# Kernel optimization log

Measured on AMD Instinct MI355X. Metric: run time of the kernel, lower is better.

## Reference

```python
import jax, jax.numpy as jnp
import numpy as np
from jax import lax


def _conv(x, w, stride=1):
    # x: [N,C,H,W], w: [O,I,k,k]
    return lax.conv_general_dilated(x, w, (stride, stride), 'SAME',
                                    dimension_numbers=('NCHW', 'OIHW', 'NCHW'))


def _up2(x):
    return jnp.repeat(jnp.repeat(x, 2, axis=-2), 2, axis=-1)


def _model(x, Wbs, bbs, Wc1, bc1, Wc2, bc2, Wes, bes):
    h = x
    for W, b in zip(Wbs, bbs):
        h = jax.nn.relu(_conv(h, W, 2) + b[None, :, None, None])
    feats = h  # [B, 512, 4, 4]
    pooled = feats.mean(axis=(2, 3))  # AdaptiveAvgPool2d((1,1)) + Flatten
    hidden = jax.nn.relu(pooled @ Wc1.T + bc1)
    logits = hidden @ Wc2.T + bc2  # [B, 5]
    cls = jnp.argmax(logits, axis=1)  # per-sample expert routing (force_class=None path)

    def expert(f, ws, bs):  # f: [512,4,4]; one sample through its routed UNet decoder
        e = f[None]
        for i in range(5):
            e = _up2(e)
            e = jax.nn.relu(_conv(e, ws[i]) + bs[i][None, :, None, None])
        e = _conv(e, ws[5]) + bs[5][None, :, None, None]  # 1x1 head -> 5 seg channels
        return e[0]

    # MoE-style dispatch: gather each sample's expert weights, then vmap (no per-sample Python loop)
    ws_sel = tuple(W[cls] for W in Wes)  # each [B, co, ci, k, k]
    bs_sel = tuple(b[cls] for b in bes)  # each [B, co]
    seg = jax.vmap(expert)(feats, ws_sel, bs_sel)  # [B, 5, 128, 128]
    return logits, cls, seg


def setup_inputs() -> dict:
    key = jax.random.key(0)
    ks = iter(jax.random.split(key, 48))

    def rn(shape):
        return jax.random.normal(next(ks), shape, dtype=jnp.float32) * 0.05

    B, E = 64, 5
    inp = {"x": jax.random.normal(next(ks), (B, 3, 128, 128), dtype=jnp.float32)}
    for i, (ci, co) in enumerate([(3, 64), (64, 128), (128, 256), (256, 512), (512, 512)], 1):
        inp[f"Wb{i}"] = rn((co, ci, 3, 3))
        inp[f"bb{i}"] = rn((co,))
    inp["Wc1"] = rn((128, 512)); inp["bc1"] = rn((128,))
    inp["Wc2"] = rn((5, 128)); inp["bc2"] = rn((5,))
    for i, (ci, co, k) in enumerate([(512, 256, 3), (256, 128, 3), (128, 64, 3),
                                     (64, 32, 3), (32, 16, 3), (16, 5, 1)], 1):
        inp[f"We{i}"] = rn((E, co, ci, k, k))
        inp[f"be{i}"] = rn((E, co))
    return inp


def reference(x, Wb1, bb1, Wb2, bb2, Wb3, bb3, Wb4, bb4, Wb5, bb5,
              Wc1, bc1, Wc2, bc2,
              We1, be1, We2, be2, We3, be3, We4, be4, We5, be5, We6, be6):
    return _model(x,
                  (Wb1, Wb2, Wb3, Wb4, Wb5), (bb1, bb2, bb3, bb4, bb5),
                  Wc1, bc1, Wc2, bc2,
                  (We1, We2, We3, We4, We5, We6), (be1, be2, be3, be4, be5, be6))
```

## Files before the change

kernel.cpp:

```cpp
#include <hip/hip_runtime.h>
#include <hip/hip_bf16.h>


typedef __attribute__((ext_vector_type(8))) short bf16x8;
typedef __attribute__((ext_vector_type(4))) float f32x4;

static __device__ __forceinline__ unsigned short f2bf(float f) {
    __hip_bfloat16 h = __float2bfloat16(f);
    return *reinterpret_cast<unsigned short*>(&h);
}
static __device__ __forceinline__ float bf2f(unsigned short u) {
    return __uint_as_float(((unsigned int)u) << 16);
}

__global__ __launch_bounds__(256)
void conv1_kernel(const float* __restrict__ in, const float* __restrict__ W,
                  const float* __restrict__ Bias,
                  unsigned short* __restrict__ out_hi,
                  unsigned short* __restrict__ out_lo)
{
    constexpr int R = 17, C = 17;
    __shared__ float ilds[3*R*C];
    __shared__ float wlds[27*32];
    const int n = blockIdx.z, co0 = blockIdx.y*32;
    const int ty = blockIdx.x >> 3, tx = blockIdx.x & 7;
    const int oh0 = ty*8, ow0 = tx*8;
    const int t = threadIdx.x, p = t & 63, grp = t >> 6;
    const int py = p >> 3, px = p & 7;
    const int r0 = 2*oh0, c0 = 2*ow0;

    const float* ibase = in + (long)n*3*16384;
    for (int idx = t; idx < 3*R*C; idx += 256) {
        int ck = idx/(R*C), rc = idx%(R*C);
        int r = rc/C, c = rc%C;
        int ih = r0+r, iw = c0+c;
        float v = 0.f;
        if (ih < 128 && iw < 128) v = ibase[ck*16384 + ih*128 + iw];
        ilds[idx] = v;
    }
    for (int idx = t; idx < 32*27; idx += 256) {
        int co = idx & 31, rem = idx >> 5;
        wlds[rem*32 + co] = W[(co0+co)*27 + rem];
    }
    __syncthreads();

    float acc[8];
    #pragma unroll
    for (int i=0;i<8;i++) acc[i]=0.f;

    #pragma unroll
    for (int ck = 0; ck < 3; ++ck) {
        float xv[9];
        #pragma unroll
        for (int kh = 0; kh < 3; ++kh)
            #pragma unroll
            for (int kw = 0; kw < 3; ++kw)
                xv[kh*3+kw] = ilds[ck*289 + (2*py+kh)*17 + 2*px+kw];
        #pragma unroll
        for (int k = 0; k < 9; ++k) {
            #pragma unroll
            for (int g = 0; g < 2; ++g) {
                const float4 w = *reinterpret_cast<const float4*>(
                    &wlds[(ck*9+k)*32 + grp*8 + g*4]);
                acc[g*4+0] += xv[k]*w.x;
                acc[g*4+1] += xv[k]*w.y;
                acc[g*4+2] += xv[k]*w.z;
                acc[g*4+3] += xv[k]*w.w;
            }
        }
    }

    const long obase = (((long)n*64 + oh0+py)*64 + ow0+px)*64 + co0 + grp*8;
    #pragma unroll
    for (int g = 0; g < 2; ++g) {
        ushort4 sh, sl;
        #pragma unroll
        for (int j = 0; j < 4; ++j) {
            int co = co0 + grp*8 + g*4 + j;
            float v = fmaxf(acc[g*4+j] + Bias[co], 0.f);
            unsigned short h = f2bf(v);
            ((unsigned short*)&sh)[j] = h;
            ((unsigned short*)&sl)[j] = f2bf(v - bf2f(h));
        }
        *reinterpret_cast<ushort4*>(&out_hi[obase + g*4]) = sh;
        *reinterpret_cast<ushort4*>(&out_lo[obase + g*4]) = sl;
    }
}

template<int CI,int CO,int HO,int NW,int NPACK>
__global__ __launch_bounds__(NW*64, 2)
void bb_conv_v2(const unsigned short* __restrict__ in_hi,
                const unsigned short* __restrict__ in_lo,
                const unsigned short* __restrict__ Whi,
                const unsigned short* __restrict__ Wlo,
                const float* __restrict__ Bias,
                unsigned short* __restrict__ out_hi,
                unsigned short* __restrict__ out_lo)
{
    constexpr int HI = HO*2;
    constexpr int TH = (NPACK==1) ? 8 : 4;
    constexpr int TW = TH;
    constexpr int R  = 2*TH+1, C = 2*TW+1;
    constexpr int CK = 32;
    constexpr int PITCH = CK + 8;
    constexpr int CO_T  = NW*64;
    constexpr int NTHR  = NW*64;

    __shared__ __align__(16) unsigned short hi_lds[NPACK*R*C*PITCH];
    __shared__ __align__(16) unsigned short lo_lds[NPACK*R*C*PITCH];

    const int n0  = blockIdx.z * NPACK;
    const int co0 = blockIdx.y * CO_T;
    constexpr int TILES_X = (NPACK==1) ? (HO/TW) : 1;
    const int ty = blockIdx.x / TILES_X, tx = blockIdx.x % TILES_X;
    const int oh0 = ty*TH, ow0 = tx*TW;
    const int r0 = 2*oh0, c0 = 2*ow0;

    const int t = threadIdx.x;
    const int w = t >> 6, lane = t & 63;
    const int s = lane & 15, q = lane >> 4;

    int dyy[4], dxx[4], tb[4];
    #pragma unroll
    for (int si = 0; si < 4; ++si) {
        if (NPACK == 1) { dyy[si] = si*2 + (s>>3); dxx[si] = s & 7; tb[si] = 0; }
        else            { dyy[si] = s >> 2;        dxx[si] = s & 3; tb[si] = si*R*C*PITCH; }
    }

    int wrow[4];
    #pragma unroll
    for (int tn = 0; tn < 4; ++tn)
        wrow[tn] = (co0 + w*64 + tn*16 + s)*9*CI + q*8;

    f32x4 acc[4][4];
    #pragma unroll
    for (int si = 0; si < 4; ++si)
        #pragma unroll
        for (int tn = 0; tn < 4; ++tn)
            acc[si][tn] = (f32x4){0.f,0.f,0.f,0.f};

    for (int ci0 = 0; ci0 < CI; ci0 += CK) {
        constexpr int C8  = CK/8;
        constexpr int PXW = R*C*C8;
        for (int i8 = t; i8 < NPACK*PXW; i8 += NTHR) {
            int ti = i8 / PXW, rem = i8 % PXW;
            int pix = rem / C8, cs = rem % C8;
            int r = pix / C, c = pix % C;
            int ih = r0 + r, iw = c0 + c;
            uint4 vh = {0u,0u,0u,0u}, vl = {0u,0u,0u,0u};
            if (ih < HI && iw < HI) {
                long off = (((long)(n0+ti)*HI + ih)*HI + iw)*CI + ci0 + cs*8;
                vh = *reinterpret_cast<const uint4*>(&in_hi[off]);
                vl = *reinterpret_cast<const uint4*>(&in_lo[off]);
            }
            *reinterpret_cast<uint4*>(&hi_lds[(ti*R*C + pix)*PITCH + cs*8]) = vh;
            *reinterpret_cast<uint4*>(&lo_lds[(ti*R*C + pix)*PITCH + cs*8]) = vl;
        }
        __syncthreads();

        bf16x8 ah[2][4], al[2][4];
        #pragma unroll
        for (int tn = 0; tn < 4; ++tn) {
            const int wo = wrow[tn] + ci0;
            ah[0][tn] = *reinterpret_cast<const bf16x8*>(&Whi[wo]);
            al[0][tn] = *reinterpret_cast<const bf16x8*>(&Wlo[wo]);
        }
        #pragma unroll
        for (int k = 0; k < 9; ++k) {
            const int cur = k & 1, nxt = cur ^ 1;
            if (k < 8) {
                #pragma unroll
                for (int tn = 0; tn < 4; ++tn) {
                    const int wo = wrow[tn] + (k+1)*CI + ci0;
                    ah[nxt][tn] = *reinterpret_cast<const bf16x8*>(&Whi[wo]);
                    al[nxt][tn] = *reinterpret_cast<const bf16x8*>(&Wlo[wo]);
                }
            }
            const int kh = k/3, kw = k%3;
            bf16x8 bh[4], bl[4];
            #pragma unroll
            for (int si = 0; si < 4; ++si) {
                const int pi = tb[si] + ((2*dyy[si]+kh)*C + 2*dxx[si]+kw)*PITCH + q*8;
                bh[si] = *reinterpret_cast<const bf16x8*>(&hi_lds[pi]);
                bl[si] = *reinterpret_cast<const bf16x8*>(&lo_lds[pi]);
            }
            #pragma unroll
            for (int si = 0; si < 4; ++si)
                #pragma unroll
                for (int tn = 0; tn < 4; ++tn) {
                    acc[si][tn] = __builtin_amdgcn_mfma_f32_16x16x32_bf16(ah[cur][tn], bh[si], acc[si][tn], 0,0,0);
                    acc[si][tn] = __builtin_amdgcn_mfma_f32_16x16x32_bf16(ah[cur][tn], bl[si], acc[si][tn], 0,0,0);
                    acc[si][tn] = __builtin_amdgcn_mfma_f32_16x16x32_bf16(al[cur][tn], bh[si], acc[si][tn], 0,0,0);
                }
        }
        __syncthreads();
    }

    #pragma unroll
    for (int si = 0; si < 4; ++si) {
        const int n_s = (NPACK==1) ? n0 : (n0 + si);
        const int oh  = (NPACK==1) ? (oh0 + dyy[si]) : dyy[si];
        const int ow  = (NPACK==1) ? (ow0 + dxx[si]) : dxx[si];
        #pragma unroll
        for (int tn = 0; tn < 4; ++tn) {
            int co_b = co0 + w*64 + tn*16 + q*4;
            ushort4 sh, sl;
            #pragma unroll
            for (int r = 0; r < 4; ++r) {
                float v = fmaxf(acc[si][tn][r] + Bias[co_b + r], 0.f);
                unsigned short h = f2bf(v);
                ((unsigned short*)&sh)[r] = h;
                ((unsigned short*)&sl)[r] = f2bf(v - bf2f(h));
            }
            long ob = (((long)n_s*HO + oh)*HO + ow)*CO + co_b;
            *reinterpret_cast<ushort4*>(&out_hi[ob]) = sh;
            *reinterpret_cast<ushort4*>(&out_lo[ob]) = sl;
        }
    }
}

__global__ __launch_bounds__(128, 2)
void conv5_partial(const unsigned short* __restrict__ in_hi,
                   const unsigned short* __restrict__ in_lo,
                   const unsigned short* __restrict__ Whi,
                   const unsigned short* __restrict__ Wlo,
                   float* __restrict__ skbuf)
{
    constexpr int CI = 512, HI = 8;
    constexpr int R = 9, C = 9, CK = 32, PITCH = 40;
    constexpr int SK = 8, CIB = CI/SK;

    __shared__ __align__(16) unsigned short hi_lds[4*R*C*PITCH];
    __shared__ __align__(16) unsigned short lo_lds[4*R*C*PITCH];

    const int sk  = blockIdx.x;
    const int co0 = blockIdx.y * 128;
    const int n0  = blockIdx.z * 4;
    const int t = threadIdx.x;
    const int w = t >> 6, lane = t & 63;
    const int s = lane & 15, q = lane >> 4;
    const int dyy = s >> 2, dxx = s & 3;

    int wrow[4];
    #pragma unroll
    for (int tn = 0; tn < 4; ++tn)
        wrow[tn] = (co0 + w*64 + tn*16 + s)*9*CI + q*8;

    f32x4 acc[4][4];
    #pragma unroll
    for (int si = 0; si < 4; ++si)
        #pragma unroll
        for (int tn = 0; tn < 4; ++tn)
            acc[si][tn] = (f32x4){0.f,0.f,0.f,0.f};

    for (int cc = 0; cc < CIB; cc += CK) {
        const int ci0 = sk*CIB + cc;
        constexpr int C8 = CK/8;
        constexpr int PXW = R*C*C8;
        for (int i8 = t; i8 < 4*PXW; i8 += 128) {
            int ti = i8 / PXW, rem = i8 % PXW;
            int pix = rem / C8, cs = rem % C8;
            int r = pix / C, c = pix % C;
            uint4 vh = {0u,0u,0u,0u}, vl = {0u,0u,0u,0u};
            if (r < HI && c < HI) {
                long off = (((long)(n0+ti)*HI + r)*HI + c)*CI + ci0 + cs*8;
                vh = *reinterpret_cast<const uint4*>(&in_hi[off]);
                vl = *reinterpret_cast<const uint4*>(&in_lo[off]);
            }
            *reinterpret_cast<uint4*>(&hi_lds[(ti*R*C + pix)*PITCH + cs*8]) = vh;
            *reinterpret_cast<uint4*>(&lo_lds[(ti*R*C + pix)*PITCH + cs*8]) = vl;
        }
        __syncthreads();

        bf16x8 ah[2][4], al[2][4];
        #pragma unroll
        for (int tn = 0; tn < 4; ++tn) {
            const int wo = wrow[tn] + ci0;
            ah[0][tn] = *reinterpret_cast<const bf16x8*>(&Whi[wo]);
            al[0][tn] = *reinterpret_cast<const bf16x8*>(&Wlo[wo]);
        }
        #pragma unroll
        for (int k = 0; k < 9; ++k) {
            const int cur = k & 1, nxt = cur ^ 1;
            if (k < 8) {
                #pragma unroll
                for (int tn = 0; tn < 4; ++tn) {
                    const int wo = wrow[tn] + (k+1)*CI + ci0;
                    ah[nxt][tn] = *reinterpret_cast<const bf16x8*>(&Whi[wo]);
                    al[nxt][tn] = *reinterpret_cast<const bf16x8*>(&Wlo[wo]);
                }
            }
            const int kh = k/3, kw = k%3;
            bf16x8 bh[4], bl[4];
            #pragma unroll
            for (int si = 0; si < 4; ++si) {
                const int pi = si*R*C*PITCH + ((2*dyy+kh)*C + 2*dxx+kw)*PITCH + q*8;
                bh[si] = *reinterpret_cast<const bf16x8*>(&hi_lds[pi]);
                bl[si] = *reinterpret_cast<const bf16x8*>(&lo_lds[pi]);
            }
            #pragma unroll
            for (int si = 0; si < 4; ++si)
                #pragma unroll
                for (int tn = 0; tn < 4; ++tn) {
                    acc[si][tn] = __builtin_amdgcn_mfma_f32_16x16x32_bf16(ah[cur][tn], bh[si], acc[si][tn], 0,0,0);
                    acc[si][tn] = __builtin_amdgcn_mfma_f32_16x16x32_bf16(ah[cur][tn], bl[si], acc[si][tn], 0,0,0);
                    acc[si][tn] = __builtin_amdgcn_mfma_f32_16x16x32_bf16(al[cur][tn], bh[si], acc[si][tn], 0,0,0);
                }
        }
        __syncthreads();
    }

    #pragma unroll
    for (int si = 0; si < 4; ++si) {
        #pragma unroll
        for (int tn = 0; tn < 4; ++tn) {
            int co_b = co0 + w*64 + tn*16 + q*4;
            long o = (((long)sk*64 + n0+si)*16 + s)*512 + co_b;
            *reinterpret_cast<f32x4*>(&skbuf[o]) = acc[si][tn];
        }
    }
}

__global__ __launch_bounds__(256)
void conv5_reduce(const float* __restrict__ skbuf, const float* __restrict__ Bias,
                  unsigned short* __restrict__ fhi, unsigned short* __restrict__ flo)
{
    int i = blockIdx.x*256 + threadIdx.x;
    int co = i & 511;
    float sacc = Bias[co];
    #pragma unroll
    for (int sk = 0; sk < 8; ++sk) sacc += skbuf[sk*524288 + i];
    float v = fmaxf(sacc, 0.f);
    unsigned short h = f2bf(v);
    fhi[i] = h;
    flo[i] = f2bf(v - bf2f(h));
}

__global__ __launch_bounds__(128, 2)
void dec1_partial(const unsigned short* __restrict__ in,
                  const unsigned short* __restrict__ WT,
                  const int* __restrict__ cls_i,
                  float* __restrict__ dbuf)
{
    constexpr int CI = 512, CO = 256, HI = 4;
    constexpr int R = 6, C = 6, CK = 64, CKQ = 2, PITCH = 72;
    constexpr int SK = 4, CIB = CI/SK;

    __shared__ __align__(16) unsigned short ilds[R*C*PITCH];

    const int sk  = blockIdx.x;
    const int co0 = blockIdx.y * 128;
    const int n   = blockIdx.z;
    const int e   = cls_i[n];
    const int t = threadIdx.x;
    const int w = t >> 6, lane = t & 63;
    const int s = lane & 15, q = lane >> 4;

    const unsigned short* Wbase = WT + (long)e*CO*9*CI;
    const unsigned short* inN   = in + (long)n*HI*HI*CI;

    int dyy[4], dxx[4];
    #pragma unroll
    for (int si = 0; si < 4; ++si) { dyy[si] = si*2 + (s>>3); dxx[si] = s & 7; }

    long wrow[4];
    #pragma unroll
    for (int tn = 0; tn < 4; ++tn)
        wrow[tn] = (long)(co0 + w*64 + tn*16 + s)*9*CI + q*8;

    f32x4 acc[4][4];
    #pragma unroll
    for (int si = 0; si < 4; ++si)
        #pragma unroll
        for (int tn = 0; tn < 4; ++tn)
            acc[si][tn] = (f32x4){0.f,0.f,0.f,0.f};

    for (int cc = 0; cc < CIB; cc += CK) {
        const int ci0 = sk*CIB + cc;
        constexpr int C8 = CK/8;
        for (int i8 = t; i8 < R*C*C8; i8 += 128) {
            int pix = i8 / C8, cs = i8 % C8;
            int r = pix / C, c = pix % C;
            int ih = r - 1, iw = c - 1;
            uint4 v = {0u,0u,0u,0u};
            if (ih >= 0 && ih < HI && iw >= 0 && iw < HI)
                v = *reinterpret_cast<const uint4*>(&inN[((long)ih*HI + iw)*CI + ci0 + cs*8]);
            *reinterpret_cast<uint4*>(&ilds[pix*PITCH + cs*8]) = v;
        }
        __syncthreads();

        bf16x8 a[2][4];
        #pragma unroll
        for (int tn = 0; tn < 4; ++tn)
            a[0][tn] = *reinterpret_cast<const bf16x8*>(&Wbase[wrow[tn] + ci0]);
        #pragma unroll
        for (int st = 0; st < 9*CKQ; ++st) {
            const int cur = st & 1, nxt = cur ^ 1;
            if (st + 1 < 9*CKQ) {
                const int kp = (st+1)/CKQ, cp = (st+1)%CKQ;
                #pragma unroll
                for (int tn = 0; tn < 4; ++tn)
                    a[nxt][tn] = *reinterpret_cast<const bf16x8*>(
                        &Wbase[wrow[tn] + kp*CI + ci0 + cp*32]);
            }
            const int k = st/CKQ, ckq = st%CKQ;
            const int kh = k/3, kw = k%3;
            #pragma unroll
            for (int si = 0; si < 4; ++si) {
                const int ihr = ((dyy[si] + kh - 1) >> 1) + 1;
                const int iwr = ((dxx[si] + kw - 1) >> 1) + 1;
                bf16x8 b = *reinterpret_cast<const bf16x8*>(
                    &ilds[(ihr*C + iwr)*PITCH + ckq*32 + q*8]);
                #pragma unroll
                for (int tn = 0; tn < 4; ++tn)
                    acc[si][tn] = __builtin_amdgcn_mfma_f32_16x16x32_bf16(
                        a[cur][tn], b, acc[si][tn], 0, 0, 0);
            }
        }
        __syncthreads();
    }

    #pragma unroll
    for (int si = 0; si < 4; ++si) {
        int px = dyy[si]*8 + dxx[si];
        #pragma unroll
        for (int tn = 0; tn < 4; ++tn) {
            int co_b = co0 + w*64 + tn*16 + q*4;
            long o = (((long)sk*64 + n)*64 + px)*256 + co_b;
            *reinterpret_cast<f32x4*>(&dbuf[o]) = acc[si][tn];
        }
    }
}

__global__ __launch_bounds__(256)
void dec1_reduce(const float* __restrict__ dbuf, const float* __restrict__ be1,
                 const int* __restrict__ cls_i, unsigned short* __restrict__ P)
{
    int i = blockIdx.x*256 + threadIdx.x;
    int n = i >> 14;
    int co = i & 255;
    int e = cls_i[n];
    float sacc = be1[e*256 + co];
    #pragma unroll
    for (int sk = 0; sk < 4; ++sk) sacc += dbuf[sk*1048576 + i];
    P[i] = f2bf(fmaxf(sacc, 0.f));
}

template<int CI>
__global__ __launch_bounds__(256)
void wtrans_split_kernel(const float* __restrict__ src,
                         unsigned short* __restrict__ hi,
                         unsigned short* __restrict__ lo)
{
    __shared__ float buf[CI*9];
    const long blk = blockIdx.x;
    const float* sp = src + blk*(CI*9);
    for (int i = threadIdx.x; i < CI*9; i += 256) buf[i] = sp[i];
    __syncthreads();
    for (int i = threadIdx.x; i < CI*9; i += 256) {
        int k = i / CI, ci = i % CI;
        float v = buf[ci*9 + k];
        unsigned short h = f2bf(v);
        hi[blk*(CI*9) + i] = h;
        lo[blk*(CI*9) + i] = f2bf(v - bf2f(h));
    }
}

template<int CI>
__global__ __launch_bounds__(256)
void wtrans_kernel(const float* __restrict__ src, unsigned short* __restrict__ dst)
{
    __shared__ float buf[CI*9];
    const long blk = blockIdx.x;
    const float* sp = src + blk*(CI*9);
    for (int i = threadIdx.x; i < CI*9; i += 256) buf[i] = sp[i];
    __syncthreads();
    unsigned short* d = dst + blk*(CI*9);
    for (int i = threadIdx.x; i < CI*9; i += 256) {
        int k = i / CI, ci = i % CI;
        d[i] = f2bf(buf[ci*9 + k]);
    }
}

__global__ __launch_bounds__(256) void pool_kernel(const unsigned short* __restrict__ fh,
                                                   const unsigned short* __restrict__ fl,
                                                   float* __restrict__ pooled)
{
    int i = blockIdx.x*256 + threadIdx.x;
    if (i < 64*512) {
        int n = i >> 9, ci = i & 511;
        const unsigned short* ph = fh + (long)n*8192 + ci;
        const unsigned short* pl = fl + (long)n*8192 + ci;
        float sacc = 0.f;
        #pragma unroll
        for (int px = 0; px < 16; ++px)
            sacc += bf2f(ph[px*512]) + bf2f(pl[px*512]);
        pooled[i] = sacc * (1.f/16.f);
    }
}

__global__ __launch_bounds__(256) void fc1_kernel(const float* __restrict__ pooled,
                                                  const float* __restrict__ Wc1,
                                                  const float* __restrict__ bc1,
                                                  float* __restrict__ hidden)
{
    int i = blockIdx.x*256 + threadIdx.x;
    if (i < 64*128) {
        int n = i/128, j = i%128;
        const float* p = pooled + n*512;
        const float* w = Wc1 + j*512;
        float sacc = 0.f;
        for (int k = 0; k < 512; ++k) sacc += p[k]*w[k];
        hidden[i] = fmaxf(sacc + bc1[j], 0.f);
    }
}

__global__ __launch_bounds__(64) void fc2_kernel(const float* __restrict__ hidden,
                                                 const float* __restrict__ Wc2,
                                                 const float* __restrict__ bc2,
                                                 float* __restrict__ out,
                                                 int* __restrict__ cls_i)
{
    int n = blockIdx.x;
    int j = threadIdx.x;
    __shared__ float lg[5];
    if (j < 5) {
        const float* h = hidden + n*128;
        const float* w = Wc2 + j*128;
        float sacc = 0.f;
        for (int k = 0; k < 128; ++k) sacc += h[k]*w[k];
        sacc += bc2[j];
        out[n*5 + j] = sacc;
        lg[j] = sacc;
    }
    __syncthreads();
    if (j == 0) {
        int am = 0; float best = lg[0];
        #pragma unroll
        for (int k = 1; k < 5; ++k) if (lg[k] > best) { best = lg[k]; am = k; }
        out[320 + n] = (float)am;
        cls_i[n] = am;
    }
}

template<int CI,int CO,int HO,int NW>
__global__ __launch_bounds__(NW*64, 2)
void dec_conv_v2(const unsigned short* __restrict__ in,
                 const unsigned short* __restrict__ WT,
                 const float* __restrict__ Be,
                 const int* __restrict__ cls_i,
                 unsigned short* __restrict__ out)
{
    constexpr int HI = HO/2;
    constexpr int R = 6, C = 6;
    constexpr int CK = 64, CKQ = CK/32;
    constexpr int PITCH = CK + 8;
    constexpr int CO_T = NW*64;
    constexpr int NTHR = NW*64;

    __shared__ __align__(16) unsigned short ilds[R*C*PITCH];

    const int n = blockIdx.z;
    const int e = cls_i[n];
    const int co0 = blockIdx.y * CO_T;
    constexpr int TILES_X = HO/8;
    const int ty = blockIdx.x / TILES_X, tx = blockIdx.x % TILES_X;
    const int oh0 = ty*8, ow0 = tx*8;
    const int ih0 = oh0/2 - 1, iw0 = ow0/2 - 1;

    const int t = threadIdx.x;
    const int w = t >> 6, lane = t & 63;
    const int s = lane & 15, q = lane >> 4;

    const unsigned short* Wbase = WT + (long)e*CO*9*CI;
    const unsigned short* inN   = in + (long)n*HI*HI*CI;

    int dyy[4], dxx[4];
    #pragma unroll
    for (int si = 0; si < 4; ++si) { dyy[si] = si*2 + (s>>3); dxx[si] = s & 7; }

    long wrow[4];
    #pragma unroll
    for (int tn = 0; tn < 4; ++tn)
        wrow[tn] = (long)(co0 + w*64 + tn*16 + s)*9*CI + q*8;

    f32x4 acc[4][4];
    #pragma unroll
    for (int si = 0; si < 4; ++si)
        #pragma unroll
        for (int tn = 0; tn < 4; ++tn)
            acc[si][tn] = (f32x4){0.f,0.f,0.f,0.f};

    for (int ci0 = 0; ci0 < CI; ci0 += CK) {
        constexpr int C8 = CK/8;
        for (int i8 = t; i8 < R*C*C8; i8 += NTHR) {
            int pix = i8 / C8, cs = i8 % C8;
            int r = pix / C, c = pix % C;
            int ih = ih0 + r, iw = iw0 + c;
            uint4 v = {0u,0u,0u,0u};
            if (ih >= 0 && ih < HI && iw >= 0 && iw < HI)
                v = *reinterpret_cast<const uint4*>(&inN[((long)ih*HI + iw)*CI + ci0 + cs*8]);
            *reinterpret_cast<uint4*>(&ilds[pix*PITCH + cs*8]) = v;
        }
        __syncthreads();

        bf16x8 a[2][4];
        #pragma unroll
        for (int tn = 0; tn < 4; ++tn)
            a[0][tn] = *reinterpret_cast<const bf16x8*>(&Wbase[wrow[tn] + ci0]);
        #pragma unroll
        for (int st = 0; st < 9*CKQ; ++st) {
            const int cur = st & 1, nxt = cur ^ 1;
            if (st + 1 < 9*CKQ) {
                const int kp = (st+1)/CKQ, cp = (st+1)%CKQ;
                #pragma unroll
                for (int tn = 0; tn < 4; ++tn)
                    a[nxt][tn] = *reinterpret_cast<const bf16x8*>(
                        &Wbase[wrow[tn] + kp*CI + ci0 + cp*32]);
            }
            const int k = st/CKQ, ckq = st%CKQ;
            const int kh = k/3, kw = k%3;
            #pragma unroll
            for (int si = 0; si < 4; ++si) {
                const int ihr = ((dyy[si] + kh - 1) >> 1) + 1;
                const int iwr = ((dxx[si] + kw - 1) >> 1) + 1;
                bf16x8 b = *reinterpret_cast<const bf16x8*>(
                    &ilds[(ihr*C + iwr)*PITCH + ckq*32 + q*8]);
                #pragma unroll
                for (int tn = 0; tn < 4; ++tn)
                    acc[si][tn] = __builtin_amdgcn_mfma_f32_16x16x32_bf16(
                        a[cur][tn], b, acc[si][tn], 0, 0, 0);
            }
        }
        __syncthreads();
    }

    #pragma unroll
    for (int si = 0; si < 4; ++si) {
        int oh = oh0 + dyy[si], ow = ow0 + dxx[si];
        #pragma unroll
        for (int tn = 0; tn < 4; ++tn) {
            int co_b = co0 + w*64 + tn*16 + q*4;
            ushort4 st4;
            #pragma unroll
            for (int r = 0; r < 4; ++r) {
                float v = acc[si][tn][r] + Be[e*CO + co_b + r];
                v = fmaxf(v, 0.f);
                ((unsigned short*)&st4)[r] = f2bf(v);
            }
            *reinterpret_cast<ushort4*>(&out[(((long)n*HO + oh)*HO + ow)*CO + co_b]) = st4;
        }
    }
}

template<int CI,int CO,int HO,int TH,int TW,int CO_T,int CK>
__global__ __launch_bounds__(256, 2)
void dec_conv_kernel(const unsigned short* __restrict__ in,
                     const unsigned short* __restrict__ WT,
                     const float* __restrict__ Be,
                     const int* __restrict__ cls_i,
                     unsigned short* __restrict__ out)
{
    constexpr int HI = HO/2;
    constexpr int R = TH/2 + 2, C = TW/2 + 2;
    constexpr int PITCH = CK + 8;
    constexpr int NT = CO_T/16;
    constexpr int S  = (TH*TW)/64;
    constexpr int SXT = TW/8;
    constexpr int CKQ = CK/32;
    constexpr int NST = 9*CKQ;
    constexpr int PF  = 3;

    __shared__ __align__(16) unsigned short ilds[R*C*PITCH];

    const int n = blockIdx.z;
    const int e = cls_i[n];
    const int co0 = blockIdx.y * CO_T;
    constexpr int TILES_X = HO/TW;
    const int ty = blockIdx.x / TILES_X, tx = blockIdx.x % TILES_X;
    const int oh0 = ty*TH, ow0 = tx*TW;
    const int ih0 = oh0/2 - 1, iw0 = ow0/2 - 1;

    const int t = threadIdx.x;
    const int w = t >> 6;
    const int lane = t & 63;
    const int s = lane & 15;
    const int q = lane >> 4;

    const unsigned short* Wbase = WT + ((long)e*CO + co0)*9*CI;
    const unsigned short* inN   = in + (long)n*HI*HI*CI;

    int wrow[NT];
    #pragma unroll
    for (int tn = 0; tn < NT; ++tn)
        wrow[tn] = (tn*16 + s)*9*CI + q*8;

    f32x4 acc[S][NT];
    #pragma unroll
    for (int si = 0; si < S; ++si)
        #pragma unroll
        for (int tn = 0; tn < NT; ++tn)
            acc[si][tn] = (f32x4){0.f,0.f,0.f,0.f};

    int dy[S], dx[S];
    #pragma unroll
    for (int si = 0; si < S; ++si) {
        int sub = w + si*4;
        int sy = sub / SXT, sx = sub % SXT;
        dy[si] = sy*2 + (s >> 3);
        dx[si] = sx*8 + (s & 7);
    }

    for (int ci0 = 0; ci0 < CI; ci0 += CK) {
        constexpr int C8 = CK/8;
        for (int i8 = t; i8 < R*C*C8; i8 += 256) {
            int pix = i8 / C8, cs = i8 % C8;
            int r = pix / C, c = pix % C;
            int ih = ih0 + r, iw = iw0 + c;
            uint4 v = {0u,0u,0u,0u};
            if (ih >= 0 && ih < HI && iw >= 0 && iw < HI)
                v = *reinterpret_cast<const uint4*>(&inN[((long)ih*HI + iw)*CI + ci0 + cs*8]);
            *reinterpret_cast<uint4*>(&ilds[pix*PITCH + cs*8]) = v;
        }
        __syncthreads();

        bf16x8 a[NST][NT];
        #pragma unroll
        for (int pf = 0; pf < PF && pf < NST; ++pf)
            #pragma unroll
            for (int tn = 0; tn < NT; ++tn) {
                const int k = pf/CKQ, ckq = pf%CKQ;
                a[pf][tn] = *reinterpret_cast<const bf16x8*>(
                    &Wbase[wrow[tn] + k*CI + ci0 + ckq*32]);
            }
        #pragma unroll
        for (int st = 0; st < NST; ++st) {
            if (st + PF < NST) {
                const int kp = (st+PF)/CKQ, cp = (st+PF)%CKQ;
                #pragma unroll
                for (int tn = 0; tn < NT; ++tn)
                    a[st+PF][tn] = *reinterpret_cast<const bf16x8*>(
                        &Wbase[wrow[tn] + kp*CI + ci0 + cp*32]);
            }
            const int k = st/CKQ, ckq = st%CKQ;
            const int kh = k/3, kw = k%3;
            #pragma unroll
            for (int si = 0; si < S; ++si) {
                int ihr = ((dy[si] + kh - 1) >> 1) + 1;
                int iwr = ((dx[si] + kw - 1) >> 1) + 1;
                bf16x8 b = *reinterpret_cast<const bf16x8*>(
                    &ilds[(ihr*C + iwr)*PITCH + ckq*32 + q*8]);
                #pragma unroll
                for (int tn = 0; tn < NT; ++tn)
                    acc[si][tn] = __builtin_amdgcn_mfma_f32_16x16x32_bf16(
                        a[st][tn], b, acc[si][tn], 0, 0, 0);
            }
        }
        __syncthreads();
    }

    #pragma unroll
    for (int si = 0; si < S; ++si) {
        int oh = oh0 + dy[si], ow = ow0 + dx[si];
        #pragma unroll
        for (int tn = 0; tn < NT; ++tn) {
            int co_b = co0 + tn*16 + q*4;
            ushort4 st4;
            #pragma unroll
            for (int r = 0; r < 4; ++r) {
                float v = acc[si][tn][r] + Be[e*CO + co_b + r];
                v = fmaxf(v, 0.f);
                ((unsigned short*)&st4)[r] = f2bf(v);
            }
            *reinterpret_cast<ushort4*>(&out[(((long)n*HO + oh)*HO + ow)*CO + co_b]) = st4;
        }
    }
}

__global__ __launch_bounds__(256) void head_kernel(const unsigned short* __restrict__ d5,
                                                   const float* __restrict__ Wh,
                                                   const float* __restrict__ bh,
                                                   const int* __restrict__ cls_i,
                                                   float* __restrict__ seg)
{
    int n = blockIdx.y;
    int p = blockIdx.x*256 + threadIdx.x;
    __shared__ float w[85];
    int e = cls_i[n];
    if (threadIdx.x < 80) w[threadIdx.x] = Wh[(long)e*80 + threadIdx.x];
    if (threadIdx.x < 5)  w[80+threadIdx.x] = bh[e*5 + threadIdx.x];
    __syncthreads();
    const unsigned short* dp = d5 + ((long)n*16384 + p)*16;
    uint4 u0 = *reinterpret_cast<const uint4*>(dp);
    uint4 u1 = *reinterpret_cast<const uint4*>(dp + 8);
    float x[16];
    unsigned int uu[4] = {u0.x, u0.y, u0.z, u0.w};
    unsigned int vv[4] = {u1.x, u1.y, u1.z, u1.w};
    #pragma unroll
    for (int i = 0; i < 4; ++i) {
        x[2*i+0] = __uint_as_float(uu[i] << 16);
        x[2*i+1] = __uint_as_float(uu[i] & 0xffff0000u);
        x[8+2*i+0] = __uint_as_float(vv[i] << 16);
        x[8+2*i+1] = __uint_as_float(vv[i] & 0xffff0000u);
    }
    #pragma unroll
    for (int co = 0; co < 5; ++co) {
        float sacc = w[80+co];
        #pragma unroll
        for (int ci = 0; ci < 16; ++ci) sacc += x[ci]*w[co*16+ci];
        seg[((long)n*5 + co)*16384 + p] = sacc;
    }
}

extern "C" void kernel_launch(void* const* d_in, const int* in_sizes, int n_in,
                              void* d_out, int out_size, void* d_ws, size_t ws_size,
                              hipStream_t stream)
{
    const float* x   = (const float*)d_in[0];
    const float* Wb1 = (const float*)d_in[1];  const float* bb1 = (const float*)d_in[2];
    const float* Wb2 = (const float*)d_in[3];  const float* bb2 = (const float*)d_in[4];
    const float* Wb3 = (const float*)d_in[5];  const float* bb3 = (const float*)d_in[6];
    const float* Wb4 = (const float*)d_in[7];  const float* bb4 = (const float*)d_in[8];
    const float* Wb5 = (const float*)d_in[9];  const float* bb5 = (const float*)d_in[10];
    const float* Wc1 = (const float*)d_in[11]; const float* bc1 = (const float*)d_in[12];
    const float* Wc2 = (const float*)d_in[13]; const float* bc2 = (const float*)d_in[14];
    const float* We1 = (const float*)d_in[15]; const float* be1 = (const float*)d_in[16];
    const float* We2 = (const float*)d_in[17]; const float* be2 = (const float*)d_in[18];
    const float* We3 = (const float*)d_in[19]; const float* be3 = (const float*)d_in[20];
    const float* We4 = (const float*)d_in[21]; const float* be4 = (const float*)d_in[22];
    const float* We5 = (const float*)d_in[23]; const float* be5 = (const float*)d_in[24];
    const float* We6 = (const float*)d_in[25]; const float* be6 = (const float*)d_in[26];

    float* out = (float*)d_out;
    char* ws = (char*)d_ws;

    unsigned short* H1hi = (unsigned short*)(ws + 0);
    unsigned short* H1lo = (unsigned short*)(ws + 33554432);
    unsigned short* H3hi = (unsigned short*)(ws + 0);
    unsigned short* H3lo = (unsigned short*)(ws + 8388608);
    unsigned short* WB4hi = (unsigned short*)(ws + 16777216);
    unsigned short* WB4lo = (unsigned short*)(ws + 19136512);
    unsigned short* WB5hi = (unsigned short*)(ws + 21495808);
    unsigned short* WB5lo = (unsigned short*)(ws + 26214400);
    float*          SKBUF5 = (float*)(ws + 0);
    unsigned short* P    = (unsigned short*)(ws + 0);
    unsigned short* Q    = (unsigned short*)(ws + 33554432);
    float*          DBUF1 = (float*)(ws + 33554432);
    unsigned short* WT1  = (unsigned short*)(ws + 50331648);
    unsigned short* WT2  = (unsigned short*)(ws + 62128128);
    unsigned short* WT3  = (unsigned short*)(ws + 65077248);
    unsigned short* WT4  = (unsigned short*)(ws + 65814528);
    unsigned short* WT5  = (unsigned short*)(ws + 65998848);

    char* Y = ws + 67108864;
    unsigned short* H2hi = (unsigned short*)(Y + 0);
    unsigned short* H2lo = (unsigned short*)(Y + 16777216);
    unsigned short* H4hi = (unsigned short*)(Y + 0);
    unsigned short* H4lo = (unsigned short*)(Y + 4194304);
    unsigned short* FShi = (unsigned short*)(Y + 8388608);
    unsigned short* FSlo = (unsigned short*)(Y + 9437184);
    float* pooled = (float*)(Y + 10485760);
    float* hidden = (float*)(Y + 10616832);
    int*   cls_i  = (int*)(Y + 10649600);

    char* W23 = ws + 100663296;
    unsigned short* WB2hi = (unsigned short*)(W23 + 0);
    unsigned short* WB2lo = (unsigned short*)(W23 + 147456);
    unsigned short* WB3hi = (unsigned short*)(W23 + 294912);
    unsigned short* WB3lo = (unsigned short*)(W23 + 884736);

    hipLaunchKernelGGL((wtrans_split_kernel<64>),  dim3(128), dim3(256), 0, stream, Wb2, WB2hi, WB2lo);
    hipLaunchKernelGGL((wtrans_split_kernel<128>), dim3(256), dim3(256), 0, stream, Wb3, WB3hi, WB3lo);

    hipLaunchKernelGGL(conv1_kernel, dim3(64,2,64), dim3(256), 0, stream, x, Wb1, bb1, H1hi, H1lo);

    hipLaunchKernelGGL((bb_conv_v2<64,128,32,2,1>), dim3(16,1,64), dim3(128), 0, stream,
                       H1hi, H1lo, WB2hi, WB2lo, bb2, H2hi, H2lo);

    hipLaunchKernelGGL((wtrans_split_kernel<256>), dim3(512), dim3(256), 0, stream, Wb4, WB4hi, WB4lo);
    hipLaunchKernelGGL((wtrans_split_kernel<512>), dim3(512), dim3(256), 0, stream, Wb5, WB5hi, WB5lo);
    hipLaunchKernelGGL((wtrans_kernel<512>), dim3(5*256), dim3(256), 0, stream, We1, WT1);
    hipLaunchKernelGGL((wtrans_kernel<256>), dim3(5*128), dim3(256), 0, stream, We2, WT2);
    hipLaunchKernelGGL((wtrans_kernel<128>), dim3(5*64),  dim3(256), 0, stream, We3, WT3);
    hipLaunchKernelGGL((wtrans_kernel<64>),  dim3(5*32),  dim3(256), 0, stream, We4, WT4);
    hipLaunchKernelGGL((wtrans_kernel<32>),  dim3(5*16),  dim3(256), 0, stream, We5, WT5);

    hipLaunchKernelGGL((bb_conv_v2<128,256,16,2,1>), dim3(4,2,64), dim3(128), 0, stream,
                       H2hi, H2lo, WB3hi, WB3lo, bb3, H3hi, H3lo);
    hipLaunchKernelGGL((bb_conv_v2<256,512, 8,2,1>), dim3(1,4,64), dim3(128), 0, stream,
                       H3hi, H3lo, WB4hi, WB4lo, bb4, H4hi, H4lo);

    hipLaunchKernelGGL(conv5_partial, dim3(8,4,16), dim3(128), 0, stream,
                       H4hi, H4lo, WB5hi, WB5lo, SKBUF5);
    hipLaunchKernelGGL(conv5_reduce, dim3(2048), dim3(256), 0, stream,
                       SKBUF5, bb5, FShi, FSlo);

    hipLaunchKernelGGL(pool_kernel, dim3(128), dim3(256), 0, stream, FShi, FSlo, pooled);
    hipLaunchKernelGGL(fc1_kernel,  dim3(32),  dim3(256), 0, stream, pooled, Wc1, bc1, hidden);
    hipLaunchKernelGGL(fc2_kernel,  dim3(64),  dim3(64),  0, stream, hidden, Wc2, bc2, out, cls_i);

    hipLaunchKernelGGL(dec1_partial, dim3(4,2,64), dim3(128), 0, stream,
                       FShi, WT1, cls_i, DBUF1);
    hipLaunchKernelGGL(dec1_reduce, dim3(4096), dim3(256), 0, stream,
                       DBUF1, be1, cls_i, P);

    hipLaunchKernelGGL((dec_conv_v2<256,128, 16,2>), dim3(4, 1,64), dim3(128), 0, stream, P, WT2, be2, cls_i, Q);
    hipLaunchKernelGGL((dec_conv_v2<128, 64, 32,1>), dim3(16,1,64), dim3(64),  0, stream, Q, WT3, be3, cls_i, P);
    hipLaunchKernelGGL((dec_conv_kernel< 64, 32, 64, 16,16, 32,64>), dim3(16, 1,64), dim3(256), 0, stream, P, WT4, be4, cls_i, Q);
    hipLaunchKernelGGL((dec_conv_kernel< 32, 16,128, 16,16, 16,32>), dim3(64, 1,64), dim3(256), 0, stream, Q, WT5, be5, cls_i, P);

    hipLaunchKernelGGL(head_kernel, dim3(64,64), dim3(256), 0, stream, P, We6, be6, cls_i, out + 384);
}
```

Measured before the change: 689.7 us.

## Restage split-bf16 convs, fuse weight transforms and classifier, retune decoder tiles

The backbone convs now stage the hi and lo activation halves through a single LDS buffer in two passes, not both halves at once. This halves shared memory and the per-k LDS reads, at the cost of extra barriers and re-loading the hi weights. The many weight-transform launches and the pool/fc1/fc2 chain are merged into a few combined kernels to cut launch overhead. The decoder convs move to a 3-slot rotating weight prefetch ring to reduce register pressure, and the last decoder conv uses a wider tile with half as many blocks.

```diff
diff --git a/kernel.cpp b/kernel.cpp
--- a/kernel.cpp
+++ b/kernel.cpp
@@ -87,9 +87,9 @@
     }
 }
 
-template<int CI,int CO,int HO,int NW,int NPACK>
+template<int CI,int CO,int HO,int NW>
 __global__ __launch_bounds__(NW*64, 2)
-void bb_conv_v2(const unsigned short* __restrict__ in_hi,
+void bb_conv_v3(const unsigned short* __restrict__ in_hi,
                 const unsigned short* __restrict__ in_lo,
                 const unsigned short* __restrict__ Whi,
                 const unsigned short* __restrict__ Wlo,
@@ -98,34 +98,29 @@
                 unsigned short* __restrict__ out_lo)
 {
     constexpr int HI = HO*2;
-    constexpr int TH = (NPACK==1) ? 8 : 4;
-    constexpr int TW = TH;
-    constexpr int R  = 2*TH+1, C = 2*TW+1;
-    constexpr int CK = 32;
-    constexpr int PITCH = CK + 8;
-    constexpr int CO_T  = NW*64;
-    constexpr int NTHR  = NW*64;
-
-    __shared__ __align__(16) unsigned short hi_lds[NPACK*R*C*PITCH];
-    __shared__ __align__(16) unsigned short lo_lds[NPACK*R*C*PITCH];
-
-    const int n0  = blockIdx.z * NPACK;
-    const int co0 = blockIdx.y * CO_T;
-    constexpr int TILES_X = (NPACK==1) ? (HO/TW) : 1;
+    constexpr int R = 17, C = 17;
+    constexpr int CK = 32, PITCH = 40;
+    constexpr int NTHR = NW*64;
+
+    __shared__ __align__(16) unsigned short xlds[R*C*PITCH];
+
+    const int n   = blockIdx.z;
+    const int co0 = blockIdx.y * (NW*64);
+    constexpr int TILES_X = HO/8;
     const int ty = blockIdx.x / TILES_X, tx = blockIdx.x % TILES_X;
-    const int oh0 = ty*TH, ow0 = tx*TW;
+    const int oh0 = ty*8, ow0 = tx*8;
     const int r0 = 2*oh0, c0 = 2*ow0;
 
     const int t = threadIdx.x;
     const int w = t >> 6, lane = t & 63;
     const int s = lane & 15, q = lane >> 4;
 
-    int dyy[4], dxx[4], tb[4];
-    #pragma unroll
-    for (int si = 0; si < 4; ++si) {
-        if (NPACK == 1) { dyy[si] = si*2 + (s>>3); dxx[si] = s & 7; tb[si] = 0; }
-        else            { dyy[si] = s >> 2;        dxx[si] = s & 3; tb[si] = si*R*C*PITCH; }
-    }
+    int dyy[4], dxx[4];
+    #pragma unroll
+    for (int si = 0; si < 4; ++si) { dyy[si] = si*2 + (s>>3); dxx[si] = s & 7; }
+
+    const unsigned short* inHn = in_hi + (long)n*HI*HI*CI;
+    const unsigned short* inLn = in_lo + (long)n*HI*HI*CI;
 
     int wrow[4];
     #pragma unroll
@@ -139,68 +134,84 @@
         for (int tn = 0; tn < 4; ++tn)
             acc[si][tn] = (f32x4){0.f,0.f,0.f,0.f};
 
-    for (int ci0 = 0; ci0 < CI; ci0 += CK) {
-        constexpr int C8  = CK/8;
-        constexpr int PXW = R*C*C8;
-        for (int i8 = t; i8 < NPACK*PXW; i8 += NTHR) {
-            int ti = i8 / PXW, rem = i8 % PXW;
-            int pix = rem / C8, cs = rem % C8;
+    auto stage = [&](const unsigned short* base, int ci0) {
+        for (int i8 = t; i8 < R*C*4; i8 += NTHR) {
+            int pix = i8 >> 2, cs = i8 & 3;
             int r = pix / C, c = pix % C;
             int ih = r0 + r, iw = c0 + c;
-            uint4 vh = {0u,0u,0u,0u}, vl = {0u,0u,0u,0u};
-            if (ih < HI && iw < HI) {
-                long off = (((long)(n0+ti)*HI + ih)*HI + iw)*CI + ci0 + cs*8;
-                vh = *reinterpret_cast<const uint4*>(&in_hi[off]);
-                vl = *reinterpret_cast<const uint4*>(&in_lo[off]);
-            }
-            *reinterpret_cast<uint4*>(&hi_lds[(ti*R*C + pix)*PITCH + cs*8]) = vh;
-            *reinterpret_cast<uint4*>(&lo_lds[(ti*R*C + pix)*PITCH + cs*8]) = vl;
-        }
-        __syncthreads();
-
-        bf16x8 ah[2][4], al[2][4];
-        #pragma unroll
-        for (int tn = 0; tn < 4; ++tn) {
-            const int wo = wrow[tn] + ci0;
-            ah[0][tn] = *reinterpret_cast<const bf16x8*>(&Whi[wo]);
-            al[0][tn] = *reinterpret_cast<const bf16x8*>(&Wlo[wo]);
-        }
-        #pragma unroll
-        for (int k = 0; k < 9; ++k) {
-            const int cur = k & 1, nxt = cur ^ 1;
-            if (k < 8) {
+            uint4 v = {0u,0u,0u,0u};
+            if (ih < HI && iw < HI)
+                v = *reinterpret_cast<const uint4*>(&base[((long)ih*HI + iw)*CI + ci0 + cs*8]);
+            *reinterpret_cast<uint4*>(&xlds[pix*PITCH + cs*8]) = v;
+        }
+    };
+
+    for (int ci0 = 0; ci0 < CI; ci0 += CK) {
+        stage(inHn, ci0);
+        __syncthreads();
+        {
+            bf16x8 ah[2][4], al[2][4];
+            #pragma unroll
+            for (int tn = 0; tn < 4; ++tn) {
+                ah[0][tn] = *reinterpret_cast<const bf16x8*>(&Whi[wrow[tn] + ci0]);
+                al[0][tn] = *reinterpret_cast<const bf16x8*>(&Wlo[wrow[tn] + ci0]);
+            }
+            #pragma unroll
+            for (int k = 0; k < 9; ++k) {
+                const int cur = k & 1, nxt = cur ^ 1;
+                if (k < 8) {
+                    #pragma unroll
+                    for (int tn = 0; tn < 4; ++tn) {
+                        ah[nxt][tn] = *reinterpret_cast<const bf16x8*>(&Whi[wrow[tn] + (k+1)*CI + ci0]);
+                        al[nxt][tn] = *reinterpret_cast<const bf16x8*>(&Wlo[wrow[tn] + (k+1)*CI + ci0]);
+                    }
+                }
+                const int kh = k/3, kw = k%3;
                 #pragma unroll
-                for (int tn = 0; tn < 4; ++tn) {
-                    const int wo = wrow[tn] + (k+1)*CI + ci0;
-                    ah[nxt][tn] = *reinterpret_cast<const bf16x8*>(&Whi[wo]);
-                    al[nxt][tn] = *reinterpret_cast<const bf16x8*>(&Wlo[wo]);
+                for (int si = 0; si < 4; ++si) {
+                    bf16x8 b = *reinterpret_cast<const bf16x8*>(
+                        &xlds[((2*dyy[si]+kh)*C + 2*dxx[si]+kw)*PITCH + q*8]);
+                    #pragma unroll
+                    for (int tn = 0; tn < 4; ++tn) {
+                        acc[si][tn] = __builtin_amdgcn_mfma_f32_16x16x32_bf16(ah[cur][tn], b, acc[si][tn], 0,0,0);
+                        acc[si][tn] = __builtin_amdgcn_mfma_f32_16x16x32_bf16(al[cur][tn], b, acc[si][tn], 0,0,0);
+                    }
                 }
             }
-            const int kh = k/3, kw = k%3;
-            bf16x8 bh[4], bl[4];
-            #pragma unroll
-            for (int si = 0; si < 4; ++si) {
-                const int pi = tb[si] + ((2*dyy[si]+kh)*C + 2*dxx[si]+kw)*PITCH + q*8;
-                bh[si] = *reinterpret_cast<const bf16x8*>(&hi_lds[pi]);
-                bl[si] = *reinterpret_cast<const bf16x8*>(&lo_lds[pi]);
-            }
-            #pragma unroll
-            for (int si = 0; si < 4; ++si)
+        }
+        __syncthreads();
+        stage(inLn, ci0);
+        __syncthreads();
+        {
+            bf16x8 a2[2][4];
+            #pragma unroll
+            for (int tn = 0; tn < 4; ++tn)
+                a2[0][tn] = *reinterpret_cast<const bf16x8*>(&Whi[wrow[tn] + ci0]);
+            #pragma unroll
+            for (int k = 0; k < 9; ++k) {
+                const int cur = k & 1, nxt = cur ^ 1;
+                if (k < 8) {
+                    #pragma unroll
+                    for (int tn = 0; tn < 4; ++tn)
+                        a2[nxt][tn] = *reinterpret_cast<const bf16x8*>(&Whi[wrow[tn] + (k+1)*CI + ci0]);
+                }
+                const int kh = k/3, kw = k%3;
                 #pragma unroll
-                for (int tn = 0; tn < 4; ++tn) {
-                    acc[si][tn] = __builtin_amdgcn_mfma_f32_16x16x32_bf16(ah[cur][tn], bh[si], acc[si][tn], 0,0,0);
-                    acc[si][tn] = __builtin_amdgcn_mfma_f32_16x16x32_bf16(ah[cur][tn], bl[si], acc[si][tn], 0,0,0);
-                    acc[si][tn] = __builtin_amdgcn_mfma_f32_16x16x32_bf16(al[cur][tn], bh[si], acc[si][tn], 0,0,0);
+                for (int si = 0; si < 4; ++si) {
+                    bf16x8 b = *reinterpret_cast<const bf16x8*>(
+                        &xlds[((2*dyy[si]+kh)*C + 2*dxx[si]+kw)*PITCH + q*8]);
+                    #pragma unroll
+                    for (int tn = 0; tn < 4; ++tn)
+                        acc[si][tn] = __builtin_amdgcn_mfma_f32_16x16x32_bf16(a2[cur][tn], b, acc[si][tn], 0,0,0);
                 }
+            }
         }
         __syncthreads();
     }
 
     #pragma unroll
     for (int si = 0; si < 4; ++si) {
-        const int n_s = (NPACK==1) ? n0 : (n0 + si);
-        const int oh  = (NPACK==1) ? (oh0 + dyy[si]) : dyy[si];
-        const int ow  = (NPACK==1) ? (ow0 + dxx[si]) : dxx[si];
+        const int oh = oh0 + dyy[si], ow = ow0 + dxx[si];
         #pragma unroll
         for (int tn = 0; tn < 4; ++tn) {
             int co_b = co0 + w*64 + tn*16 + q*4;
@@ -212,7 +223,7 @@
                 ((unsigned short*)&sh)[r] = h;
                 ((unsigned short*)&sl)[r] = f2bf(v - bf2f(h));
             }
-            long ob = (((long)n_s*HO + oh)*HO + ow)*CO + co_b;
+            long ob = (((long)n*HO + oh)*HO + ow)*CO + co_b;
             *reinterpret_cast<ushort4*>(&out_hi[ob]) = sh;
             *reinterpret_cast<ushort4*>(&out_lo[ob]) = sl;
         }
@@ -228,10 +239,8 @@
 {
     constexpr int CI = 512, HI = 8;
     constexpr int R = 9, C = 9, CK = 32, PITCH = 40;
-    constexpr int SK = 8, CIB = CI/SK;
-
-    __shared__ __align__(16) unsigned short hi_lds[4*R*C*PITCH];
-    __shared__ __align__(16) unsigned short lo_lds[4*R*C*PITCH];
+
+    __shared__ __align__(16) unsigned short xlds[4*R*C*PITCH];
 
     const int sk  = blockIdx.x;
     const int co0 = blockIdx.y * 128;
@@ -253,59 +262,79 @@
         for (int tn = 0; tn < 4; ++tn)
             acc[si][tn] = (f32x4){0.f,0.f,0.f,0.f};
 
-    for (int cc = 0; cc < CIB; cc += CK) {
-        const int ci0 = sk*CIB + cc;
-        constexpr int C8 = CK/8;
-        constexpr int PXW = R*C*C8;
-        for (int i8 = t; i8 < 4*PXW; i8 += 128) {
-            int ti = i8 / PXW, rem = i8 % PXW;
-            int pix = rem / C8, cs = rem % C8;
+    auto stage = [&](const unsigned short* base, int ci0) {
+        for (int i8 = t; i8 < 4*324; i8 += 128) {
+            int ti = i8 / 324, rem = i8 % 324;
+            int pix = rem >> 2, cs = rem & 3;
             int r = pix / C, c = pix % C;
-            uint4 vh = {0u,0u,0u,0u}, vl = {0u,0u,0u,0u};
-            if (r < HI && c < HI) {
-                long off = (((long)(n0+ti)*HI + r)*HI + c)*CI + ci0 + cs*8;
-                vh = *reinterpret_cast<const uint4*>(&in_hi[off]);
-                vl = *reinterpret_cast<const uint4*>(&in_lo[off]);
-            }
-            *reinterpret_cast<uint4*>(&hi_lds[(ti*R*C + pix)*PITCH + cs*8]) = vh;
-            *reinterpret_cast<uint4*>(&lo_lds[(ti*R*C + pix)*PITCH + cs*8]) = vl;
-        }
-        __syncthreads();
-
-        bf16x8 ah[2][4], al[2][4];
-        #pragma unroll
-        for (int tn = 0; tn < 4; ++tn) {
-            const int wo = wrow[tn] + ci0;
-            ah[0][tn] = *reinterpret_cast<const bf16x8*>(&Whi[wo]);
-            al[0][tn] = *reinterpret_cast<const bf16x8*>(&Wlo[wo]);
-        }
-        #pragma unroll
-        for (int k = 0; k < 9; ++k) {
-            const int cur = k & 1, nxt = cur ^ 1;
-            if (k < 8) {
+            uint4 v = {0u,0u,0u,0u};
+            if (r < HI && c < HI)
+                v = *reinterpret_cast<const uint4*>(
+                    &base[(((long)(n0+ti)*HI + r)*HI + c)*CI + ci0 + cs*8]);
+            *reinterpret_cast<uint4*>(&xlds[(ti*R*C + pix)*PITCH + cs*8]) = v;
+        }
+    };
+
+    for (int cc = 0; cc < 64; cc += CK) {
+        const int ci0 = sk*64 + cc;
+        stage(in_hi, ci0);
+        __syncthreads();
+        {
+            bf16x8 ah[2][4], al[2][4];
+            #pragma unroll
+            for (int tn = 0; tn < 4; ++tn) {
+                ah[0][tn] = *reinterpret_cast<const bf16x8*>(&Whi[wrow[tn] + ci0]);
+                al[0][tn] = *reinterpret_cast<const bf16x8*>(&Wlo[wrow[tn] + ci0]);
+            }
+            #pragma unroll
+            for (int k = 0; k < 9; ++k) {
+                const int cur = k & 1, nxt = cur ^ 1;
+                if (k < 8) {
+                    #pragma unroll
+                    for (int tn = 0; tn < 4; ++tn) {
+                        ah[nxt][tn] = *reinterpret_cast<const bf16x8*>(&Whi[wrow[tn] + (k+1)*CI + ci0]);
+                        al[nxt][tn] = *reinterpret_cast<const bf16x8*>(&Wlo[wrow[tn] + (k+1)*CI + ci0]);
+                    }
+                }
+                const int kh = k/3, kw = k%3;
                 #pragma unroll
-                for (int tn = 0; tn < 4; ++tn) {
-                    const int wo = wrow[tn] + (k+1)*CI + ci0;
-                    ah[nxt][tn] = *reinterpret_cast<const bf16x8*>(&Whi[wo]);
-                    al[nxt][tn] = *reinterpret_cast<const bf16x8*>(&Wlo[wo]);
+                for (int si = 0; si < 4; ++si) {
+                    bf16x8 b = *reinterpret_cast<const bf16x8*>(
+                        &xlds[(si*R*C + (2*dyy+kh)*C + 2*dxx+kw)*PITCH + q*8]);
+                    #pragma unroll
+                    for (int tn = 0; tn < 4; ++tn) {
+                        acc[si][tn] = __builtin_amdgcn_mfma_f32_16x16x32_bf16(ah[cur][tn], b, acc[si][tn], 0,0,0);
+                        acc[si][tn] = __builtin_amdgcn_mfma_f32_16x16x32_bf16(al[cur][tn], b, acc[si][tn], 0,0,0);
+                    }
                 }
             }
-            const int kh = k/3, kw = k%3;
-            bf16x8 bh[4], bl[4];
-            #pragma unroll
-            for (int si = 0; si < 4; ++si) {
-                const int pi = si*R*C*PITCH + ((2*dyy+kh)*C + 2*dxx+kw)*PITCH + q*8;
-                bh[si] = *reinterpret_cast<const bf16x8*>(&hi_lds[pi]);
-                bl[si] = *reinterpret_cast<const bf16x8*>(&lo_lds[pi]);
-            }
-            #pragma unroll
-            for (int si = 0; si < 4; ++si)
+        }
+        __syncthreads();
+        stage(in_lo, ci0);
+        __syncthreads();
+        {
+            bf16x8 a2[2][4];
+            #pragma unroll
+            for (int tn = 0; tn < 4; ++tn)
+                a2[0][tn] = *reinterpret_cast<const bf16x8*>(&Whi[wrow[tn] + ci0]);
+            #pragma unroll
+            for (int k = 0; k < 9; ++k) {
+                const int cur = k & 1, nxt = cur ^ 1;
+                if (k < 8) {
+                    #pragma unroll
+                    for (int tn = 0; tn < 4; ++tn)
+                        a2[nxt][tn] = *reinterpret_cast<const bf16x8*>(&Whi[wrow[tn] + (k+1)*CI + ci0]);
+                }
+                const int kh = k/3, kw = k%3;
                 #pragma unroll
-                for (int tn = 0; tn < 4; ++tn) {
-                    acc[si][tn] = __builtin_amdgcn_mfma_f32_16x16x32_bf16(ah[cur][tn], bh[si], acc[si][tn], 0,0,0);
-                    acc[si][tn] = __builtin_amdgcn_mfma_f32_16x16x32_bf16(ah[cur][tn], bl[si], acc[si][tn], 0,0,0);
-                    acc[si][tn] = __builtin_amdgcn_mfma_f32_16x16x32_bf16(al[cur][tn], bh[si], acc[si][tn], 0,0,0);
+                for (int si = 0; si < 4; ++si) {
+                    bf16x8 b = *reinterpret_cast<const bf16x8*>(
+                        &xlds[(si*R*C + (2*dyy+kh)*C + 2*dxx+kw)*PITCH + q*8]);
+                    #pragma unroll
+                    for (int tn = 0; tn < 4; ++tn)
+                        acc[si][tn] = __builtin_amdgcn_mfma_f32_16x16x32_bf16(a2[cur][tn], b, acc[si][tn], 0,0,0);
                 }
+            }
         }
         __syncthreads();
     }
@@ -344,7 +373,7 @@
 {
     constexpr int CI = 512, CO = 256, HI = 4;
     constexpr int R = 6, C = 6, CK = 64, CKQ = 2, PITCH = 72;
-    constexpr int SK = 4, CIB = CI/SK;
+    constexpr int NST = 9*CKQ;
 
     __shared__ __align__(16) unsigned short ilds[R*C*PITCH];
 
@@ -375,11 +404,10 @@
         for (int tn = 0; tn < 4; ++tn)
             acc[si][tn] = (f32x4){0.f,0.f,0.f,0.f};
 
-    for (int cc = 0; cc < CIB; cc += CK) {
-        const int ci0 = sk*CIB + cc;
-        constexpr int C8 = CK/8;
-        for (int i8 = t; i8 < R*C*C8; i8 += 128) {
-            int pix = i8 / C8, cs = i8 % C8;
+    for (int cc = 0; cc < CI/4; cc += CK) {
+        const int ci0 = sk*(CI/4) + cc;
+        for (int i8 = t; i8 < R*C*8; i8 += 128) {
+            int pix = i8 >> 3, cs = i8 & 7;
             int r = pix / C, c = pix % C;
             int ih = r - 1, iw = c - 1;
             uint4 v = {0u,0u,0u,0u};
@@ -389,19 +417,25 @@
         }
         __syncthreads();
 
-        bf16x8 a[2][4];
-        #pragma unroll
-        for (int tn = 0; tn < 4; ++tn)
-            a[0][tn] = *reinterpret_cast<const bf16x8*>(&Wbase[wrow[tn] + ci0]);
-        #pragma unroll
-        for (int st = 0; st < 9*CKQ; ++st) {
-            const int cur = st & 1, nxt = cur ^ 1;
-            if (st + 1 < 9*CKQ) {
-                const int kp = (st+1)/CKQ, cp = (st+1)%CKQ;
+        bf16x8 a[3][4];
+        #pragma unroll
+        for (int pf = 0; pf < 3; ++pf) {
+            const int kp = pf/CKQ, cp = pf%CKQ;
+            #pragma unroll
+            for (int tn = 0; tn < 4; ++tn)
+                a[pf][tn] = *reinterpret_cast<const bf16x8*>(&Wbase[wrow[tn] + kp*CI + ci0 + cp*32]);
+        }
+        #pragma unroll
+        for (int st = 0; st < NST; ++st) {
+            const int slot = st % 3;
+            bf16x8 acur[4];
+            #pragma unroll
+            for (int tn = 0; tn < 4; ++tn) acur[tn] = a[slot][tn];
+            if (st + 3 < NST) {
+                const int kp = (st+3)/CKQ, cp = (st+3)%CKQ;
                 #pragma unroll
                 for (int tn = 0; tn < 4; ++tn)
-                    a[nxt][tn] = *reinterpret_cast<const bf16x8*>(
-                        &Wbase[wrow[tn] + kp*CI + ci0 + cp*32]);
+                    a[slot][tn] = *reinterpret_cast<const bf16x8*>(&Wbase[wrow[tn] + kp*CI + ci0 + cp*32]);
             }
             const int k = st/CKQ, ckq = st%CKQ;
             const int kh = k/3, kw = k%3;
@@ -413,8 +447,7 @@
                     &ilds[(ihr*C + iwr)*PITCH + ckq*32 + q*8]);
                 #pragma unroll
                 for (int tn = 0; tn < 4; ++tn)
-                    acc[si][tn] = __builtin_amdgcn_mfma_f32_16x16x32_bf16(
-                        a[cur][tn], b, acc[si][tn], 0, 0, 0);
+                    acc[si][tn] = __builtin_amdgcn_mfma_f32_16x16x32_bf16(acur[tn], b, acc[si][tn], 0, 0, 0);
             }
         }
         __syncthreads();
@@ -447,94 +480,109 @@
 }
 
 template<int CI>
-__global__ __launch_bounds__(256)
-void wtrans_split_kernel(const float* __restrict__ src,
-                         unsigned short* __restrict__ hi,
-                         unsigned short* __restrict__ lo)
-{
-    __shared__ float buf[CI*9];
-    const long blk = blockIdx.x;
-    const float* sp = src + blk*(CI*9);
-    for (int i = threadIdx.x; i < CI*9; i += 256) buf[i] = sp[i];
+__device__ __forceinline__ void trans_split_row(const float* __restrict__ src,
+                                                unsigned short* __restrict__ hi,
+                                                unsigned short* __restrict__ lo,
+                                                int blk, float* buf, int t)
+{
+    const float* sp = src + (long)blk*(CI*9);
+    for (int i = t; i < CI*9; i += 256) buf[i] = sp[i];
     __syncthreads();
-    for (int i = threadIdx.x; i < CI*9; i += 256) {
+    for (int i = t; i < CI*9; i += 256) {
         int k = i / CI, ci = i % CI;
         float v = buf[ci*9 + k];
         unsigned short h = f2bf(v);
-        hi[blk*(CI*9) + i] = h;
-        lo[blk*(CI*9) + i] = f2bf(v - bf2f(h));
+        hi[(long)blk*(CI*9) + i] = h;
+        lo[(long)blk*(CI*9) + i] = f2bf(v - bf2f(h));
     }
 }
 
 template<int CI>
+__device__ __forceinline__ void trans_row(const float* __restrict__ src,
+                                          unsigned short* __restrict__ dst,
+                                          int blk, float* buf, int t)
+{
+    const float* sp = src + (long)blk*(CI*9);
+    for (int i = t; i < CI*9; i += 256) buf[i] = sp[i];
+    __syncthreads();
+    for (int i = t; i < CI*9; i += 256) {
+        int k = i / CI, ci = i % CI;
+        dst[(long)blk*(CI*9) + i] = f2bf(buf[ci*9 + k]);
+    }
+}
+
 __global__ __launch_bounds__(256)
-void wtrans_kernel(const float* __restrict__ src, unsigned short* __restrict__ dst)
-{
-    __shared__ float buf[CI*9];
-    const long blk = blockIdx.x;
-    const float* sp = src + blk*(CI*9);
-    for (int i = threadIdx.x; i < CI*9; i += 256) buf[i] = sp[i];
-    __syncthreads();
-    unsigned short* d = dst + blk*(CI*9);
-    for (int i = threadIdx.x; i < CI*9; i += 256) {
-        int k = i / CI, ci = i % CI;
-        d[i] = f2bf(buf[ci*9 + k]);
-    }
-}
-
-__global__ __launch_bounds__(256) void pool_kernel(const unsigned short* __restrict__ fh,
-                                                   const unsigned short* __restrict__ fl,
-                                                   float* __restrict__ pooled)
-{
-    int i = blockIdx.x*256 + threadIdx.x;
-    if (i < 64*512) {
-        int n = i >> 9, ci = i & 511;
+void early_trans_kernel(const float* __restrict__ Wb2, const float* __restrict__ Wb3,
+                        unsigned short* __restrict__ WB2hi, unsigned short* __restrict__ WB2lo,
+                        unsigned short* __restrict__ WB3hi, unsigned short* __restrict__ WB3lo)
+{
+    __shared__ float buf[128*9];
+    int b = blockIdx.x, t = threadIdx.x;
+    if (b < 128) trans_split_row<64>(Wb2, WB2hi, WB2lo, b, buf, t);
+    else         trans_split_row<128>(Wb3, WB3hi, WB3lo, b-128, buf, t);
+}
+
+__global__ __launch_bounds__(256)
+void late_trans_kernel(const float* __restrict__ Wb4, const float* __restrict__ Wb5,
+                       const float* __restrict__ We1, const float* __restrict__ We2,
+                       const float* __restrict__ We3, const float* __restrict__ We4,
+                       const float* __restrict__ We5,
+                       unsigned short* __restrict__ WB4hi, unsigned short* __restrict__ WB4lo,
+                       unsigned short* __restrict__ WB5hi, unsigned short* __restrict__ WB5lo,
+                       unsigned short* __restrict__ WT1, unsigned short* __restrict__ WT2,
+                       unsigned short* __restrict__ WT3, unsigned short* __restrict__ WT4,
+                       unsigned short* __restrict__ WT5)
+{
+    __shared__ float buf[512*9];
+    int b = blockIdx.x, t = threadIdx.x;
+    if      (b < 512)  trans_split_row<256>(Wb4, WB4hi, WB4lo, b,      buf, t);
+    else if (b < 1024) trans_split_row<512>(Wb5, WB5hi, WB5lo, b-512,  buf, t);
+    else if (b < 2304) trans_row<512>(We1, WT1, b-1024, buf, t);
+    else if (b < 2944) trans_row<256>(We2, WT2, b-2304, buf, t);
+    else if (b < 3264) trans_row<128>(We3, WT3, b-2944, buf, t);
+    else if (b < 3424) trans_row<64> (We4, WT4, b-3264, buf, t);
+    else               trans_row<32> (We5, WT5, b-3424, buf, t);
+}
+
+__global__ __launch_bounds__(128)
+void classifier_kernel(const unsigned short* __restrict__ fh,
+                       const unsigned short* __restrict__ fl,
+                       const float* __restrict__ Wc1, const float* __restrict__ bc1,
+                       const float* __restrict__ Wc2, const float* __restrict__ bc2,
+                       float* __restrict__ out, int* __restrict__ cls_i)
+{
+    __shared__ float pooled[512];
+    __shared__ float hidden[128];
+    __shared__ float lg[5];
+    const int n = blockIdx.x, t = threadIdx.x;
+
+    for (int ci = t; ci < 512; ci += 128) {
         const unsigned short* ph = fh + (long)n*8192 + ci;
         const unsigned short* pl = fl + (long)n*8192 + ci;
         float sacc = 0.f;
         #pragma unroll
         for (int px = 0; px < 16; ++px)
             sacc += bf2f(ph[px*512]) + bf2f(pl[px*512]);
-        pooled[i] = sacc * (1.f/16.f);
-    }
-}
-
-__global__ __launch_bounds__(256) void fc1_kernel(const float* __restrict__ pooled,
-                                                  const float* __restrict__ Wc1,
-                                                  const float* __restrict__ bc1,
-                                                  float* __restrict__ hidden)
-{
-    int i = blockIdx.x*256 + threadIdx.x;
-    if (i < 64*128) {
-        int n = i/128, j = i%128;
-        const float* p = pooled + n*512;
-        const float* w = Wc1 + j*512;
+        pooled[ci] = sacc * (1.f/16.f);
+    }
+    __syncthreads();
+    {
+        const float* w = Wc1 + t*512;
         float sacc = 0.f;
-        for (int k = 0; k < 512; ++k) sacc += p[k]*w[k];
-        hidden[i] = fmaxf(sacc + bc1[j], 0.f);
-    }
-}
-
-__global__ __launch_bounds__(64) void fc2_kernel(const float* __restrict__ hidden,
-                                                 const float* __restrict__ Wc2,
-                                                 const float* __restrict__ bc2,
-                                                 float* __restrict__ out,
-                                                 int* __restrict__ cls_i)
-{
-    int n = blockIdx.x;
-    int j = threadIdx.x;
-    __shared__ float lg[5];
-    if (j < 5) {
-        const float* h = hidden + n*128;
-        const float* w = Wc2 + j*128;
+        for (int k = 0; k < 512; ++k) sacc += pooled[k]*w[k];
+        hidden[t] = fmaxf(sacc + bc1[t], 0.f);
+    }
+    __syncthreads();
+    if (t < 5) {
+        const float* w = Wc2 + t*128;
         float sacc = 0.f;
-        for (int k = 0; k < 128; ++k) sacc += h[k]*w[k];
-        sacc += bc2[j];
-        out[n*5 + j] = sacc;
-        lg[j] = sacc;
+        for (int k = 0; k < 128; ++k) sacc += hidden[k]*w[k];
+        sacc += bc2[t];
+        out[n*5 + t] = sacc;
+        lg[t] = sacc;
     }
     __syncthreads();
-    if (j == 0) {
+    if (t == 0) {
         int am = 0; float best = lg[0];
         #pragma unroll
         for (int k = 1; k < 5; ++k) if (lg[k] > best) { best = lg[k]; am = k; }
@@ -555,14 +603,14 @@
     constexpr int R = 6, C = 6;
     constexpr int CK = 64, CKQ = CK/32;
     constexpr int PITCH = CK + 8;
-    constexpr int CO_T = NW*64;
     constexpr int NTHR = NW*64;
+    constexpr int NST = 9*CKQ;
 
     __shared__ __align__(16) unsigned short ilds[R*C*PITCH];
 
     const int n = blockIdx.z;
     const int e = cls_i[n];
-    const int co0 = blockIdx.y * CO_T;
+    const int co0 = blockIdx.y * (NW*64);
     constexpr int TILES_X = HO/8;
     const int ty = blockIdx.x / TILES_X, tx = blockIdx.x % TILES_X;
     const int oh0 = ty*8, ow0 = tx*8;
@@ -592,9 +640,8 @@
             acc[si][tn] = (f32x4){0.f,0.f,0.f,0.f};
 
     for (int ci0 = 0; ci0 < CI; ci0 += CK) {
-        constexpr int C8 = CK/8;
-        for (int i8 = t; i8 < R*C*C8; i8 += NTHR) {
-            int pix = i8 / C8, cs = i8 % C8;
+        for (int i8 = t; i8 < R*C*8; i8 += NTHR) {
+            int pix = i8 >> 3, cs = i8 & 7;
             int r = pix / C, c = pix % C;
             int ih = ih0 + r, iw = iw0 + c;
             uint4 v = {0u,0u,0u,0u};
@@ -604,19 +651,25 @@
         }
         __syncthreads();
 
-        bf16x8 a[2][4];
-        #pragma unroll
-        for (int tn = 0; tn < 4; ++tn)
-            a[0][tn] = *reinterpret_cast<const bf16x8*>(&Wbase[wrow[tn] + ci0]);
-        #pragma unroll
-        for (int st = 0; st < 9*CKQ; ++st) {
-            const int cur = st & 1, nxt = cur ^ 1;
-            if (st + 1 < 9*CKQ) {
-                const int kp = (st+1)/CKQ, cp = (st+1)%CKQ;
+        bf16x8 a[3][4];
+        #pragma unroll
+        for (int pf = 0; pf < 3; ++pf) {
+            const int kp = pf/CKQ, cp = pf%CKQ;
+            #pragma unroll
+            for (int tn = 0; tn < 4; ++tn)
+                a[pf][tn] = *reinterpret_cast<const bf16x8*>(&Wbase[wrow[tn] + kp*CI + ci0 + cp*32]);
+        }
+        #pragma unroll
+        for (int st = 0; st < NST; ++st) {
+            const int slot = st % 3;
+            bf16x8 acur[4];
+            #pragma unroll
+            for (int tn = 0; tn < 4; ++tn) acur[tn] = a[slot][tn];
+            if (st + 3 < NST) {
+                const int kp = (st+3)/CKQ, cp = (st+3)%CKQ;
                 #pragma unroll
                 for (int tn = 0; tn < 4; ++tn)
-                    a[nxt][tn] = *reinterpret_cast<const bf16x8*>(
-                        &Wbase[wrow[tn] + kp*CI + ci0 + cp*32]);
+                    a[slot][tn] = *reinterpret_cast<const bf16x8*>(&Wbase[wrow[tn] + kp*CI + ci0 + cp*32]);
             }
             const int k = st/CKQ, ckq = st%CKQ;
             const int kh = k/3, kw = k%3;
@@ -628,8 +681,7 @@
                     &ilds[(ihr*C + iwr)*PITCH + ckq*32 + q*8]);
                 #pragma unroll
                 for (int tn = 0; tn < 4; ++tn)
-                    acc[si][tn] = __builtin_amdgcn_mfma_f32_16x16x32_bf16(
-                        a[cur][tn], b, acc[si][tn], 0, 0, 0);
+                    acc[si][tn] = __builtin_amdgcn_mfma_f32_16x16x32_bf16(acur[tn], b, acc[si][tn], 0, 0, 0);
             }
         }
         __syncthreads();
@@ -669,7 +721,6 @@
     constexpr int SXT = TW/8;
     constexpr int CKQ = CK/32;
     constexpr int NST = 9*CKQ;
-    constexpr int PF  = 3;
 
     __shared__ __align__(16) unsigned short ilds[R*C*PITCH];
 
@@ -690,10 +741,10 @@
     const unsigned short* Wbase = WT + ((long)e*CO + co0)*9*CI;
     const unsigned short* inN   = in + (long)n*HI*HI*CI;
 
-    int wrow[NT];
+    long wrow[NT];
     #pragma unroll
     for (int tn = 0; tn < NT; ++tn)
-        wrow[tn] = (tn*16 + s)*9*CI + q*8;
+        wrow[tn] = (long)(tn*16 + s)*9*CI + q*8;
 
     f32x4 acc[S][NT];
     #pragma unroll
@@ -724,23 +775,25 @@
         }
         __syncthreads();
 
-        bf16x8 a[NST][NT];
-        #pragma unroll
-        for (int pf = 0; pf < PF && pf < NST; ++pf)
-            #pragma unroll
-            for (int tn = 0; tn < NT; ++tn) {
-                const int k = pf/CKQ, ckq = pf%CKQ;
-                a[pf][tn] = *reinterpret_cast<const bf16x8*>(
-                    &Wbase[wrow[tn] + k*CI + ci0 + ckq*32]);
-            }
+        bf16x8 a[3][NT];
+        #pragma unroll
+        for (int pf = 0; pf < 3 && pf < NST; ++pf) {
+            const int kp = pf/CKQ, cp = pf%CKQ;
+            #pragma unroll
+            for (int tn = 0; tn < NT; ++tn)
+                a[pf][tn] = *reinterpret_cast<const bf16x8*>(&Wbase[wrow[tn] + kp*CI + ci0 + cp*32]);
+        }
         #pragma unroll
         for (int st = 0; st < NST; ++st) {
-            if (st + PF < NST) {
-                const int kp = (st+PF)/CKQ, cp = (st+PF)%CKQ;
+            const int slot = st % 3;
+            bf16x8 acur[NT];
+            #pragma unroll
+            for (int tn = 0; tn < NT; ++tn) acur[tn] = a[slot][tn];
+            if (st + 3 < NST) {
+                const int kp = (st+3)/CKQ, cp = (st+3)%CKQ;
                 #pragma unroll
                 for (int tn = 0; tn < NT; ++tn)
-                    a[st+PF][tn] = *reinterpret_cast<const bf16x8*>(
-                        &Wbase[wrow[tn] + kp*CI + ci0 + cp*32]);
+                    a[slot][tn] = *reinterpret_cast<const bf16x8*>(&Wbase[wrow[tn] + kp*CI + ci0 + cp*32]);
             }
             const int k = st/CKQ, ckq = st%CKQ;
             const int kh = k/3, kw = k%3;
@@ -752,8 +805,7 @@
                     &ilds[(ihr*C + iwr)*PITCH + ckq*32 + q*8]);
                 #pragma unroll
                 for (int tn = 0; tn < NT; ++tn)
-                    acc[si][tn] = __builtin_amdgcn_mfma_f32_16x16x32_bf16(
-                        a[st][tn], b, acc[si][tn], 0, 0, 0);
+                    acc[si][tn] = __builtin_amdgcn_mfma_f32_16x16x32_bf16(acur[tn], b, acc[si][tn], 0, 0, 0);
             }
         }
         __syncthreads();
@@ -859,8 +911,6 @@
     unsigned short* H4lo = (unsigned short*)(Y + 4194304);
     unsigned short* FShi = (unsigned short*)(Y + 8388608);
     unsigned short* FSlo = (unsigned short*)(Y + 9437184);
-    float* pooled = (float*)(Y + 10485760);
-    float* hidden = (float*)(Y + 10616832);
     int*   cls_i  = (int*)(Y + 10649600);
 
     char* W23 = ws + 100663296;
@@ -869,25 +919,21 @@
     unsigned short* WB3hi = (unsigned short*)(W23 + 294912);
     unsigned short* WB3lo = (unsigned short*)(W23 + 884736);
 
-    hipLaunchKernelGGL((wtrans_split_kernel<64>),  dim3(128), dim3(256), 0, stream, Wb2, WB2hi, WB2lo);
-    hipLaunchKernelGGL((wtrans_split_kernel<128>), dim3(256), dim3(256), 0, stream, Wb3, WB3hi, WB3lo);
+    hipLaunchKernelGGL(early_trans_kernel, dim3(384), dim3(256), 0, stream,
+                       Wb2, Wb3, WB2hi, WB2lo, WB3hi, WB3lo);
 
     hipLaunchKernelGGL(conv1_kernel, dim3(64,2,64), dim3(256), 0, stream, x, Wb1, bb1, H1hi, H1lo);
 
-    hipLaunchKernelGGL((bb_conv_v2<64,128,32,2,1>), dim3(16,1,64), dim3(128), 0, stream,
+    hipLaunchKernelGGL((bb_conv_v3<64,128,32,2>), dim3(16,1,64), dim3(128), 0, stream,
                        H1hi, H1lo, WB2hi, WB2lo, bb2, H2hi, H2lo);
 
-    hipLaunchKernelGGL((wtrans_split_kernel<256>), dim3(512), dim3(256), 0, stream, Wb4, WB4hi, WB4lo);
-    hipLaunchKernelGGL((wtrans_split_kernel<512>), dim3(512), dim3(256), 0, stream, Wb5, WB5hi, WB5lo);
-    hipLaunchKernelGGL((wtrans_kernel<512>), dim3(5*256), dim3(256), 0, stream, We1, WT1);
-    hipLaunchKernelGGL((wtrans_kernel<256>), dim3(5*128), dim3(256), 0, stream, We2, WT2);
-    hipLaunchKernelGGL((wtrans_kernel<128>), dim3(5*64),  dim3(256), 0, stream, We3, WT3);
-    hipLaunchKernelGGL((wtrans_kernel<64>),  dim3(5*32),  dim3(256), 0, stream, We4, WT4);
-    hipLaunchKernelGGL((wtrans_kernel<32>),  dim3(5*16),  dim3(256), 0, stream, We5, WT5);
-
-    hipLaunchKernelGGL((bb_conv_v2<128,256,16,2,1>), dim3(4,2,64), dim3(128), 0, stream,
+    hipLaunchKernelGGL(late_trans_kernel, dim3(3504), dim3(256), 0, stream,
+                       Wb4, Wb5, We1, We2, We3, We4, We5,
+                       WB4hi, WB4lo, WB5hi, WB5lo, WT1, WT2, WT3, WT4, WT5);
+
+    hipLaunchKernelGGL((bb_conv_v3<128,256,16,2>), dim3(4,2,64), dim3(128), 0, stream,
                        H2hi, H2lo, WB3hi, WB3lo, bb3, H3hi, H3lo);
-    hipLaunchKernelGGL((bb_conv_v2<256,512, 8,2,1>), dim3(1,4,64), dim3(128), 0, stream,
+    hipLaunchKernelGGL((bb_conv_v3<256,512, 8,2>), dim3(1,4,64), dim3(128), 0, stream,
                        H3hi, H3lo, WB4hi, WB4lo, bb4, H4hi, H4lo);
 
     hipLaunchKernelGGL(conv5_partial, dim3(8,4,16), dim3(128), 0, stream,
@@ -895,9 +941,8 @@
     hipLaunchKernelGGL(conv5_reduce, dim3(2048), dim3(256), 0, stream,
                        SKBUF5, bb5, FShi, FSlo);
 
-    hipLaunchKernelGGL(pool_kernel, dim3(128), dim3(256), 0, stream, FShi, FSlo, pooled);
-    hipLaunchKernelGGL(fc1_kernel,  dim3(32),  dim3(256), 0, stream, pooled, Wc1, bc1, hidden);
-    hipLaunchKernelGGL(fc2_kernel,  dim3(64),  dim3(64),  0, stream, hidden, Wc2, bc2, out, cls_i);
+    hipLaunchKernelGGL(classifier_kernel, dim3(64), dim3(128), 0, stream,
+                       FShi, FSlo, Wc1, bc1, Wc2, bc2, out, cls_i);
 
     hipLaunchKernelGGL(dec1_partial, dim3(4,2,64), dim3(128), 0, stream,
                        FShi, WT1, cls_i, DBUF1);
@@ -907,7 +952,7 @@
     hipLaunchKernelGGL((dec_conv_v2<256,128, 16,2>), dim3(4, 1,64), dim3(128), 0, stream, P, WT2, be2, cls_i, Q);
     hipLaunchKernelGGL((dec_conv_v2<128, 64, 32,1>), dim3(16,1,64), dim3(64),  0, stream, Q, WT3, be3, cls_i, P);
     hipLaunchKernelGGL((dec_conv_kernel< 64, 32, 64, 16,16, 32,64>), dim3(16, 1,64), dim3(256), 0, stream, P, WT4, be4, cls_i, Q);
-    hipLaunchKernelGGL((dec_conv_kernel< 32, 16,128, 16,16, 16,32>), dim3(64, 1,64), dim3(256), 0, stream, Q, WT5, be5, cls_i, P);
+    hipLaunchKernelGGL((dec_conv_kernel< 32, 16,128, 16,32, 16,32>), dim3(32, 1,64), dim3(256), 0, stream, Q, WT5, be5, cls_i, P);
 
     hipLaunchKernelGGL(head_kernel, dim3(64,64), dim3(256), 0, stream, P, We6, be6, cls_i, out + 384);
 }
```

Measured after the change: 748.0 us. 8.4% more time.
